# Kernel tuning notes

Hardware: AMD Instinct MI355X
Metric: run time of the kernel (lower is better)

## Reference

```python
import jax, jax.numpy as jnp
import numpy as np

B, P, K = 2, 8192, 20
ELL = 0.15          # ell_min + ell_rand
ELL_BASE = 10.0     # ell_basedist
COLOR_SCALE = 0.2
RES_MIN = 0.1       # res_mag_min
RES_MAX = 2.0       # res_mag_max
BIG = 1e10          # masking constant for invalid db points
EPS = 1e-12


def setup_inputs() -> dict:
    key = jax.random.key(0)
    ks = jax.random.split(key, 16)
    scale = jnp.array([20.0, 20.0, 60.0], jnp.float32)
    off = jnp.array([-10.0, -10.0, 1.0], jnp.float32)  # depth z in [1, 61] m
    xyz1 = jax.random.uniform(ks[0], (B, P, 3), jnp.float32) * scale + off
    xyz2 = jax.random.uniform(ks[1], (B, P, 3), jnp.float32) * scale + off
    hsv1 = jax.random.uniform(ks[2], (B, P, 3), jnp.float32)
    hsv2 = jax.random.uniform(ks[3], (B, P, 3), jnp.float32)
    n1 = jax.random.normal(ks[4], (B, P, 3), jnp.float32)
    normal1 = n1 / jnp.linalg.norm(n1, axis=-1, keepdims=True)
    n2 = jax.random.normal(ks[5], (B, P, 3), jnp.float32)
    normal2 = n2 / jnp.linalg.norm(n2, axis=-1, keepdims=True)
    nres1 = jax.random.uniform(ks[6], (B, P, 1), jnp.float32)
    nres2 = jax.random.uniform(ks[7], (B, P, 1), jnp.float32)

    def rot(k):
        a = np.asarray(jax.random.normal(k, (B, 3, 3), jnp.float32))
        q, _ = np.linalg.qr(a)
        return jnp.asarray(q, jnp.float32)

    R12 = rot(ks[8])
    R21 = rot(ks[9])
    t12 = jax.random.normal(ks[10], (B, 3, 1), jnp.float32) * 0.5
    t21 = jax.random.normal(ks[11], (B, 3, 1), jnp.float32) * 0.5
    npts1 = jax.random.randint(ks[12], (B,), P // 2, P + 1)
    npts2 = jax.random.randint(ks[13], (B,), P // 2, P + 1)
    return dict(xyz1=xyz1, xyz2=xyz2, hsv1=hsv1, hsv2=hsv2,
                normal1=normal1, normal2=normal2, nres1=nres1, nres2=nres2,
                R12=R12, t12=t12, R21=R21, t21=t21, npts1=npts1, npts2=npts2)


def _knn(pq, pdb, len_db):
    # pq [B,Pq,3], pdb [B,Pdb,3] -> squared dists [B,Pq,K], idx [B,Pq,K]
    d2 = jnp.sum((pq[:, :, None, :] - pdb[:, None, :, :]) ** 2, axis=-1)
    valid = jnp.arange(pdb.shape[1])[None, :] < len_db[:, None]
    d2 = jnp.where(valid[:, None, :], d2, BIG)
    neg, idx = jax.lax.top_k(-d2, K)
    return -neg, idx


def _gather(f, idx):
    # f [B,Pdb,C], idx [B,Pq,K] -> [B,Pq,K,C]  (knn_gather)
    return jax.vmap(lambda fb, ib: fb[ib])(f, idx)


def _transform(xyz, normal, R, t):
    x = jnp.einsum('bij,bpj->bpi', R, xyz) + t[:, :, 0][:, None, :]
    n = jnp.einsum('bij,bpj->bpi', R, normal)
    return x, n


def _side(pq, hq, nq, rq, lq, pdb, hdb, ndb, rdb, ldb):
    dists, idx = _knn(pq, pdb, ldb)                      # [B,P,K]
    # length_scale = clamp(ell*(z-base)/base, min=ell)^2
    ls = jnp.maximum(ELL * (pq[:, :, 2:3] - ELL_BASE) / ELL_BASE, ELL) ** 2
    dist_k = jnp.exp(-dists / ls)
    hsv_knn = _gather(hdb, idx)                          # [B,P,K,3]
    cdist = jnp.sqrt(jnp.sum((hq[:, :, None, :] - hsv_knn) ** 2, -1) + EPS)
    color_k = jnp.exp(-cdist / COLOR_SCALE)
    n_knn = _gather(ndb, idx)                            # [B,P,K,3]
    r_knn = _gather(rdb, idx)                            # [B,P,K,1]
    alpha = (2 * RES_MIN / (2 * RES_MIN / RES_MAX + rq[:, :, None, :] + r_knn))[..., 0]
    normal_k = jnp.maximum(jnp.sum(nq[:, :, None, :] * n_knn, -1) * alpha, 0.0)
    mask = (jnp.arange(pq.shape[1])[None, :, None] < lq[:, None, None]).astype(dist_k.dtype)
    total = jnp.sum(dist_k * color_k * normal_k * mask)
    return total / (lq.sum().astype(dist_k.dtype) * K)


def reference(xyz1, xyz2, hsv1, hsv2, normal1, normal2, nres1, nres2,
              R12, t12, R21, t21, npts1, npts2):
    x2in1, n2in1 = _transform(xyz2, normal2, R12, t12)   # pcl_gt_2_in_1
    x1in2, n1in2 = _transform(xyz1, normal1, R21, t21)   # pcl_gt_1_in_2
    k1 = _side(xyz1, hsv1, normal1, nres1, npts1, x2in1, hsv2, n2in1, nres2, npts2)
    k2 = _side(xyz2, hsv2, normal2, nres2, npts2, x1in2, hsv1, n1in2, nres1, npts1)
    return (k1 + k2) / 2
```

## Files before the change

### kernel.cpp

```cpp
#include <hip/hip_runtime.h>
#include <cstdint>
#include <cstddef>

#define PBUF 8192
#define NZB 256
#define NYB 32
#define NBINS (NZB * NYB)
#define NCOMBO 4
#define KNN 20
#define CAP 256

#define ZMIN_F (-72.0f)
#define INV_BINW (256.0f / 144.0f)
#define INV_YBINW (32.0f / 144.0f)

#define IDX_MASK 0x1FFFu
#define D2_MASK 0xFFFFE000u
#define KEY_INF 0xFFFFFFFFu

#define THR_MULT 21.0f

#define OFF_ACCUM   0
#define OFF_DBCUR   2048
#define ZERO_BYTES  (2048 + NCOMBO * NBINS * 4)
#define OFF_DBSTART (2048 + NCOMBO * NBINS * 4)
#define OFF_DBPOS   (OFF_DBSTART + NCOMBO * (NBINS + 1) * 4)
#define ARR_BYTES   (NCOMBO * PBUF * 16)
#define OFF_DBF1    (OFF_DBPOS + ARR_BYTES)
#define OFF_DBF2    (OFF_DBF1 + ARR_BYTES)

__device__ __forceinline__ int binOfZ(float z) {
  int b = (int)floorf((z - ZMIN_F) * INV_BINW);
  return min(max(b, 0), NZB - 1);
}
__device__ __forceinline__ int binOfY(float y) {
  int b = (int)floorf((y - ZMIN_F) * INV_YBINW);
  return min(max(b, 0), NYB - 1);
}

__device__ __forceinline__ float xformRow(const float* R, float tr, float x0, float x1, float x2) {
  return __fmaf_rn(R[2], x2, __fmaf_rn(R[1], x1, __fmaf_rn(R[0], x0, tr)));
}

__global__ __launch_bounds__(256) void k_count(
    const float* xyz1, const float* xyz2,
    const float* R12, const float* t12,
    const float* R21, const float* t21,
    const int* npts1, const int* npts2, char* ws) {
  int tid = blockIdx.x * 256 + threadIdx.x;
  int c = tid >> 13, j = tid & (PBUF - 1);
  int s = c >> 1, b = c & 1;
  const float* dsrc = s == 0 ? xyz2 : xyz1;
  const float* R  = (s == 0 ? R12 : R21) + b * 9;
  const float* tt = (s == 0 ? t12 : t21) + b * 3;
  int ldb = (s == 0 ? npts2 : npts1)[b];
  if (j < ldb) {
    const float* x = dsrc + (size_t)(b * PBUF + j) * 3;
    float y1 = xformRow(R + 3, tt[1], x[0], x[1], x[2]);
    float y2 = xformRow(R + 6, tt[2], x[0], x[1], x[2]);
    int bin = binOfZ(y2) * NYB + binOfY(y1);
    atomicAdd((int*)(ws + OFF_DBCUR) + c * NBINS + bin, 1);
  }
}

__global__ __launch_bounds__(256) void k_prefix(char* ws) {
  __shared__ int sWave[4];
  const int c = blockIdx.x;
  const int t = threadIdx.x;
  const int lane = t & 63, w = t >> 6;
  int* cnt = (int*)(ws + OFF_DBCUR) + c * NBINS;
  int* st  = (int*)(ws + OFF_DBSTART) + c * (NBINS + 1);
  int vals[32];
  int base = t * 32;
  int sum = 0;
  #pragma unroll
  for (int k = 0; k < 32; ++k) { vals[k] = cnt[base + k]; sum += vals[k]; }
  int incl = sum;
  #pragma unroll
  for (int o = 1; o < 64; o <<= 1) {
    int n = __shfl_up(incl, o);
    if (lane >= o) incl += n;
  }
  if (lane == 63) sWave[w] = incl;
  __syncthreads();
  int wbase = 0;
  #pragma unroll
  for (int k = 0; k < 4; ++k) wbase += (k < w) ? sWave[k] : 0;
  int run = wbase + incl - sum;
  #pragma unroll
  for (int k = 0; k < 32; ++k) {
    st[base + k] = run;
    cnt[base + k] = run;
    run += vals[k];
  }
  if (t == 255) st[NBINS] = run;
}

__global__ __launch_bounds__(256) void k_scatter(
    const float* xyz1, const float* xyz2,
    const float* hsv1, const float* hsv2,
    const float* normal1, const float* normal2,
    const float* nres1, const float* nres2,
    const float* R12, const float* t12,
    const float* R21, const float* t21,
    const int* npts1, const int* npts2, char* ws) {
  int tid = blockIdx.x * 256 + threadIdx.x;
  int c = tid >> 13, j = tid & (PBUF - 1);
  int s = c >> 1, b = c & 1;
  size_t pj = (size_t)(b * PBUF + j);

  const float* dsrc = s == 0 ? xyz2 : xyz1;
  const float* dh = s == 0 ? hsv2 : hsv1;
  const float* dn = s == 0 ? normal2 : normal1;
  const float* dr = s == 0 ? nres2 : nres1;
  const float* R  = (s == 0 ? R12 : R21) + b * 9;
  const float* tt = (s == 0 ? t12 : t21) + b * 3;
  int ldb = (s == 0 ? npts2 : npts1)[b];
  if (j < ldb) {
    const float* x = dsrc + pj * 3;
    float y0 = xformRow(R + 0, tt[0], x[0], x[1], x[2]);
    float y1 = xformRow(R + 3, tt[1], x[0], x[1], x[2]);
    float y2 = xformRow(R + 6, tt[2], x[0], x[1], x[2]);
    const float* n = dn + pj * 3;
    float n0 = xformRow(R + 0, 0.f, n[0], n[1], n[2]);
    float n1 = xformRow(R + 3, 0.f, n[0], n[1], n[2]);
    float n2 = xformRow(R + 6, 0.f, n[0], n[1], n[2]);
    const float* h = dh + pj * 3;
    float r = dr[pj];
    int bin = binOfZ(y2) * NYB + binOfY(y1);
    int pos = atomicAdd((int*)(ws + OFF_DBCUR) + c * NBINS + bin, 1) + c * PBUF;
    ((float4*)(ws + OFF_DBPOS))[pos] = make_float4(y0, y1, y2, 0.f);
    ((float4*)(ws + OFF_DBF1))[pos] = make_float4(h[0], h[1], h[2], r);
    ((float4*)(ws + OFF_DBF2))[pos] = make_float4(n0, n1, n2, 0.f);
  }
}

__global__ __launch_bounds__(256) void k_main(
    const float* xyz1, const float* xyz2,
    const float* hsv1, const float* hsv2,
    const float* normal1, const float* normal2,
    const float* nres1, const float* nres2,
    const int* npts1, const int* npts2, char* ws) {
  __shared__ unsigned sBuf[4 * (CAP + 4)];
  const int lane = threadIdx.x & 63;
  const int wIn = threadIdx.x >> 6;
  const int gw = blockIdx.x * 4 + wIn;
  const int c = gw >> 13;
  const int qi = (int)(__brev((unsigned)(gw & 8191)) >> 19);
  const int s = c >> 1, b = c & 1;
  const int lq = (s == 0 ? npts1 : npts2)[b];
  if (qi >= lq) return;

  const size_t qo = (size_t)(b * PBUF + qi);
  const float* qx = (s == 0 ? xyz1 : xyz2) + qo * 3;
  const float* qh = (s == 0 ? hsv1 : hsv2) + qo * 3;
  const float* qn = (s == 0 ? normal1 : normal2) + qo * 3;
  const float* qr = (s == 0 ? nres1 : nres2) + qo;
  const float qpx = qx[0], qpy = qx[1], qpz = qx[2];
  const float qh0 = qh[0], qh1 = qh[1], qh2 = qh[2];
  const float qn0 = qn[0], qn1 = qn[1], qn2 = qn[2];
  const float qres = qr[0];

  const float ell = fmaxf(0.015f * (qpz - 10.0f), 0.15f);
  const float ls = ell * ell;
  const float thrF = THR_MULT * ls;
  const float rad = sqrtf(thrF);
  const float inv_ls = 1.0f / ls;

  const int* F = (const int*)(ws + OFF_DBSTART) + c * (NBINS + 1);
  const int zlo = binOfZ(qpz - rad), zhi = binOfZ(qpz + rad);
  const int ylo = binOfY(qpy - rad), yhi = binOfY(qpy + rad);
  const int nseg = zhi - zlo + 1;

  int segS = 0, segLen = 0;
  if (lane < nseg) {
    int zk = zlo + lane;
    segS = F[zk * NYB + ylo];
    segLen = F[zk * NYB + yhi + 1] - segS;
  }
  int cum = segLen;
  #pragma unroll
  for (int o = 1; o < 64; o <<= 1) {
    int n = __shfl_up(cum, o);
    if (lane >= o) cum += n;
  }
  const int L = __shfl(cum, 63);
  const int excl = cum - segLen;

  const float4* dbPos = (const float4*)(ws + OFF_DBPOS) + c * PBUF;
  const float4* dbF1  = (const float4*)(ws + OFF_DBF1) + c * PBUF;
  const float4* dbF2  = (const float4*)(ws + OFF_DBF2) + c * PBUF;

  auto computeJ = [&](int base) -> int {
    int tc = min(base + lane, L - 1);
    int kk = 0;
    #pragma unroll
    for (int step = 8; step; step >>= 1) {
      int cnd = kk + step;
      int e = __shfl(excl, cnd & 63);
      if (cnd < nseg && e <= tc) kk = cnd;
    }
    return __shfl(segS, kk) + (tc - __shfl(excl, kk));
  };

  unsigned* buf = sBuf + wIn * (CAP + 4);
  int pos = 0;
  if (L > 0) {
    int jc = computeJ(0);
    float4 pc = dbPos[jc];
    for (int base = 0; base < L; base += 64) {
      int j = jc;
      float4 p = pc;
      int nb = base + 64;
      if (nb < L) {
        jc = computeJ(nb);
        pc = dbPos[jc];
      }
      bool in = (base + lane) < L;
      float dx = p.x - qpx, dy = p.y - qpy, dz = p.z - qpz;
      float d2 = __fmaf_rn(dx, dx, __fmaf_rn(dy, dy, dz * dz));
      bool keep = in && (d2 <= thrF);
      unsigned long long m = __ballot(keep);
      int rank = (int)__popcll(m & ((1ull << lane) - 1ull));
      if (keep) {
        int pidx = pos + rank;
        if (pidx < CAP) buf[pidx] = (__float_as_uint(d2) & D2_MASK) | (unsigned)j;
      }
      pos += (int)__popcll(m);
    }
    pos = min(pos, CAP);
  }

  if (lane < 4) buf[pos + lane] = KEY_INF;
  unsigned r0 = (lane       < pos) ? buf[lane]       : KEY_INF;
  unsigned r1 = (lane + 64  < pos) ? buf[lane + 64]  : KEY_INF;
  unsigned r2 = (lane + 128 < pos) ? buf[lane + 128] : KEY_INF;
  unsigned r3 = (lane + 192 < pos) ? buf[lane + 192] : KEY_INF;
  int k0 = 0, k1 = 0, k2 = 0, k3 = 0;
  const int nch = (pos + 3) >> 2;
  const uint4* b4 = (const uint4*)buf;
  for (int ch = 0; ch < nch; ++ch) {
    uint4 q4 = b4[ch];
    k0 += (q4.x < r0) + (q4.y < r0) + (q4.z < r0) + (q4.w < r0);
    k1 += (q4.x < r1) + (q4.y < r1) + (q4.z < r1) + (q4.w < r1);
    k2 += (q4.x < r2) + (q4.y < r2) + (q4.z < r2) + (q4.w < r2);
    k3 += (q4.x < r3) + (q4.y < r3) + (q4.z < r3) + (q4.w < r3);
  }

  auto evalKey = [&](unsigned key, int rk) -> float {
    if (rk >= KNN || key == KEY_INF) return 0.f;
    int j = (int)(key & IDX_MASK);
    float4 p = dbPos[j];
    float4 f1 = dbF1[j];
    float4 f2 = dbF2[j];
    float dx = p.x - qpx, dy = p.y - qpy, dz = p.z - qpz;
    float d2 = __fmaf_rn(dx, dx, __fmaf_rn(dy, dy, dz * dz));
    float dist_k = __expf(-d2 * inv_ls);
    float c0 = qh0 - f1.x, c1 = qh1 - f1.y, c2 = qh2 - f1.z;
    float cd = sqrtf(__fmaf_rn(c0, c0, __fmaf_rn(c1, c1, c2 * c2)) + 1e-12f);
    float color_k = __expf(cd * -5.0f);
    float alpha = 0.2f / (0.1f + qres + f1.w);
    float nd = __fmaf_rn(qn0, f2.x, __fmaf_rn(qn1, f2.y, qn2 * f2.z));
    float nk = fmaxf(nd * alpha, 0.0f);
    return dist_k * color_k * nk;
  };
  float lsum = evalKey(r0, k0) + evalKey(r1, k1) + evalKey(r2, k2) + evalKey(r3, k3);

  #pragma unroll
  for (int o = 32; o; o >>= 1) lsum += __shfl_down(lsum, o);
  if (lane == 0)
    atomicAdd((float*)(ws + OFF_ACCUM) + (s * 256 + (blockIdx.x & 255)), lsum);
}

__global__ void k_final(const int* npts1, const int* npts2, const char* ws, float* out) {
  int lane = threadIdx.x;
  const float* acc = (const float*)(ws + OFF_ACCUM);
  float s1 = acc[lane] + acc[lane + 64] + acc[lane + 128] + acc[lane + 192];
  float s2 = acc[256 + lane] + acc[256 + lane + 64] + acc[256 + lane + 128] + acc[256 + lane + 192];
  #pragma unroll
  for (int o = 32; o; o >>= 1) {
    s1 += __shfl_down(s1, o);
    s2 += __shfl_down(s2, o);
  }
  if (lane == 0) {
    float k1 = s1 / (20.0f * (float)(npts1[0] + npts1[1]));
    float k2 = s2 / (20.0f * (float)(npts2[0] + npts2[1]));
    out[0] = 0.5f * (k1 + k2);
  }
}

extern "C" void kernel_launch(void* const* d_in, const int* in_sizes, int n_in,
                              void* d_out, int out_size, void* d_ws, size_t ws_size,
                              hipStream_t stream) {
  const float* xyz1 = (const float*)d_in[0];
  const float* xyz2 = (const float*)d_in[1];
  const float* hsv1 = (const float*)d_in[2];
  const float* hsv2 = (const float*)d_in[3];
  const float* normal1 = (const float*)d_in[4];
  const float* normal2 = (const float*)d_in[5];
  const float* nres1 = (const float*)d_in[6];
  const float* nres2 = (const float*)d_in[7];
  const float* R12 = (const float*)d_in[8];
  const float* t12 = (const float*)d_in[9];
  const float* R21 = (const float*)d_in[10];
  const float* t21 = (const float*)d_in[11];
  const int* npts1 = (const int*)d_in[12];
  const int* npts2 = (const int*)d_in[13];
  char* ws = (char*)d_ws;
  float* out = (float*)d_out;

  hipMemsetAsync(ws, 0, ZERO_BYTES, stream);
  k_count<<<dim3(NCOMBO * PBUF / 256), dim3(256), 0, stream>>>(
      xyz1, xyz2, R12, t12, R21, t21, npts1, npts2, ws);
  k_prefix<<<dim3(NCOMBO), dim3(256), 0, stream>>>(ws);
  k_scatter<<<dim3(NCOMBO * PBUF / 256), dim3(256), 0, stream>>>(
      xyz1, xyz2, hsv1, hsv2, normal1, normal2, nres1, nres2,
      R12, t12, R21, t21, npts1, npts2, ws);
  k_main<<<dim3(NCOMBO * PBUF / 4), dim3(256), 0, stream>>>(
      xyz1, xyz2, hsv1, hsv2, normal1, normal2, nres1, nres2, npts1, npts2, ws);
  k_final<<<dim3(1), dim3(64), 0, stream>>>(npts1, npts2, ws, out);
}
```

Before: 138.4 us.

## Replace count/prefix/scatter binning with fixed-capacity per-bin slots

Drops the count and prefix-sum kernels and scatters points straight into fixed 128-slot buckets per bin, so two launches and one pass over the points go away. The query side now builds one segment per (z,y) bin instead of one contiguous run per z row, and widens the segment search. Candidate keys grow to 64 bits because slot indices no longer fit in 13 bits, which doubles shared memory and the work of the rank-count loop. Points beyond 128 in a single bin are silently dropped.

```diff
diff --git a/kernel.cpp b/kernel.cpp
--- a/kernel.cpp
+++ b/kernel.cpp
@@ -9,23 +9,22 @@
 #define NCOMBO 4
 #define KNN 20
 #define CAP 256
+#define CAPB 128
+#define SLOTS (NBINS * CAPB)
 
 #define ZMIN_F (-72.0f)
 #define INV_BINW (256.0f / 144.0f)
 #define INV_YBINW (32.0f / 144.0f)
 
-#define IDX_MASK 0x1FFFu
-#define D2_MASK 0xFFFFE000u
-#define KEY_INF 0xFFFFFFFFu
+#define KEY_INF 0xFFFFFFFFFFFFFFFFull
 
 #define THR_MULT 21.0f
 
 #define OFF_ACCUM   0
 #define OFF_DBCUR   2048
 #define ZERO_BYTES  (2048 + NCOMBO * NBINS * 4)
-#define OFF_DBSTART (2048 + NCOMBO * NBINS * 4)
-#define OFF_DBPOS   (OFF_DBSTART + NCOMBO * (NBINS + 1) * 4)
-#define ARR_BYTES   (NCOMBO * PBUF * 16)
+#define OFF_DBPOS   ZERO_BYTES
+#define ARR_BYTES   (NCOMBO * SLOTS * 16)
 #define OFF_DBF1    (OFF_DBPOS + ARR_BYTES)
 #define OFF_DBF2    (OFF_DBF1 + ARR_BYTES)
 
@@ -40,60 +39,6 @@
 
 __device__ __forceinline__ float xformRow(const float* R, float tr, float x0, float x1, float x2) {
   return __fmaf_rn(R[2], x2, __fmaf_rn(R[1], x1, __fmaf_rn(R[0], x0, tr)));
-}
-
-__global__ __launch_bounds__(256) void k_count(
-    const float* xyz1, const float* xyz2,
-    const float* R12, const float* t12,
-    const float* R21, const float* t21,
-    const int* npts1, const int* npts2, char* ws) {
-  int tid = blockIdx.x * 256 + threadIdx.x;
-  int c = tid >> 13, j = tid & (PBUF - 1);
-  int s = c >> 1, b = c & 1;
-  const float* dsrc = s == 0 ? xyz2 : xyz1;
-  const float* R  = (s == 0 ? R12 : R21) + b * 9;
-  const float* tt = (s == 0 ? t12 : t21) + b * 3;
-  int ldb = (s == 0 ? npts2 : npts1)[b];
-  if (j < ldb) {
-    const float* x = dsrc + (size_t)(b * PBUF + j) * 3;
-    float y1 = xformRow(R + 3, tt[1], x[0], x[1], x[2]);
-    float y2 = xformRow(R + 6, tt[2], x[0], x[1], x[2]);
-    int bin = binOfZ(y2) * NYB + binOfY(y1);
-    atomicAdd((int*)(ws + OFF_DBCUR) + c * NBINS + bin, 1);
-  }
-}
-
-__global__ __launch_bounds__(256) void k_prefix(char* ws) {
-  __shared__ int sWave[4];
-  const int c = blockIdx.x;
-  const int t = threadIdx.x;
-  const int lane = t & 63, w = t >> 6;
-  int* cnt = (int*)(ws + OFF_DBCUR) + c * NBINS;
-  int* st  = (int*)(ws + OFF_DBSTART) + c * (NBINS + 1);
-  int vals[32];
-  int base = t * 32;
-  int sum = 0;
-  #pragma unroll
-  for (int k = 0; k < 32; ++k) { vals[k] = cnt[base + k]; sum += vals[k]; }
-  int incl = sum;
-  #pragma unroll
-  for (int o = 1; o < 64; o <<= 1) {
-    int n = __shfl_up(incl, o);
-    if (lane >= o) incl += n;
-  }
-  if (lane == 63) sWave[w] = incl;
-  __syncthreads();
-  int wbase = 0;
-  #pragma unroll
-  for (int k = 0; k < 4; ++k) wbase += (k < w) ? sWave[k] : 0;
-  int run = wbase + incl - sum;
-  #pragma unroll
-  for (int k = 0; k < 32; ++k) {
-    st[base + k] = run;
-    cnt[base + k] = run;
-    run += vals[k];
-  }
-  if (t == 255) st[NBINS] = run;
 }
 
 __global__ __launch_bounds__(256) void k_scatter(
@@ -118,9 +63,10 @@
   int ldb = (s == 0 ? npts2 : npts1)[b];
   if (j < ldb) {
     const float* x = dsrc + pj * 3;
-    float y0 = xformRow(R + 0, tt[0], x[0], x[1], x[2]);
-    float y1 = xformRow(R + 3, tt[1], x[0], x[1], x[2]);
-    float y2 = xformRow(R + 6, tt[2], x[0], x[1], x[2]);
+    float x0 = x[0], x1 = x[1], x2 = x[2];
+    float y0 = xformRow(R + 0, tt[0], x0, x1, x2);
+    float y1 = xformRow(R + 3, tt[1], x0, x1, x2);
+    float y2 = xformRow(R + 6, tt[2], x0, x1, x2);
     const float* n = dn + pj * 3;
     float n0 = xformRow(R + 0, 0.f, n[0], n[1], n[2]);
     float n1 = xformRow(R + 3, 0.f, n[0], n[1], n[2]);
@@ -128,10 +74,13 @@
     const float* h = dh + pj * 3;
     float r = dr[pj];
     int bin = binOfZ(y2) * NYB + binOfY(y1);
-    int pos = atomicAdd((int*)(ws + OFF_DBCUR) + c * NBINS + bin, 1) + c * PBUF;
-    ((float4*)(ws + OFF_DBPOS))[pos] = make_float4(y0, y1, y2, 0.f);
-    ((float4*)(ws + OFF_DBF1))[pos] = make_float4(h[0], h[1], h[2], r);
-    ((float4*)(ws + OFF_DBF2))[pos] = make_float4(n0, n1, n2, 0.f);
+    int slot = atomicAdd((int*)(ws + OFF_DBCUR) + c * NBINS + bin, 1);
+    if (slot < CAPB) {
+      size_t pos = (size_t)c * SLOTS + (size_t)bin * CAPB + slot;
+      ((float4*)(ws + OFF_DBPOS))[pos] = make_float4(y0, y1, y2, 0.f);
+      ((float4*)(ws + OFF_DBF1))[pos] = make_float4(h[0], h[1], h[2], r);
+      ((float4*)(ws + OFF_DBF2))[pos] = make_float4(n0, n1, n2, 0.f);
+    }
   }
 }
 
@@ -141,7 +90,7 @@
     const float* normal1, const float* normal2,
     const float* nres1, const float* nres2,
     const int* npts1, const int* npts2, char* ws) {
-  __shared__ unsigned sBuf[4 * (CAP + 4)];
+  __shared__ unsigned long long sBuf[4 * (CAP + 2)];
   const int lane = threadIdx.x & 63;
   const int wIn = threadIdx.x >> 6;
   const int gw = blockIdx.x * 4 + wIn;
@@ -167,16 +116,18 @@
   const float rad = sqrtf(thrF);
   const float inv_ls = 1.0f / ls;
 
-  const int* F = (const int*)(ws + OFF_DBSTART) + c * (NBINS + 1);
+  const int* C = (const int*)(ws + OFF_DBCUR) + c * NBINS;
   const int zlo = binOfZ(qpz - rad), zhi = binOfZ(qpz + rad);
   const int ylo = binOfY(qpy - rad), yhi = binOfY(qpy + rad);
-  const int nseg = zhi - zlo + 1;
+  const int nyw = yhi - ylo + 1;
+  const int nseg = (zhi - zlo + 1) * nyw;
 
   int segS = 0, segLen = 0;
   if (lane < nseg) {
-    int zk = zlo + lane;
-    segS = F[zk * NYB + ylo];
-    segLen = F[zk * NYB + yhi + 1] - segS;
+    int zi = lane / nyw, yi = lane - zi * nyw;
+    int bin = (zlo + zi) * NYB + (ylo + yi);
+    segS = bin * CAPB;
+    segLen = min(C[bin], CAPB);
   }
   int cum = segLen;
   #pragma unroll
@@ -187,15 +138,15 @@
   const int L = __shfl(cum, 63);
   const int excl = cum - segLen;
 
-  const float4* dbPos = (const float4*)(ws + OFF_DBPOS) + c * PBUF;
-  const float4* dbF1  = (const float4*)(ws + OFF_DBF1) + c * PBUF;
-  const float4* dbF2  = (const float4*)(ws + OFF_DBF2) + c * PBUF;
+  const float4* dbPos = (const float4*)(ws + OFF_DBPOS) + (size_t)c * SLOTS;
+  const float4* dbF1  = (const float4*)(ws + OFF_DBF1) + (size_t)c * SLOTS;
+  const float4* dbF2  = (const float4*)(ws + OFF_DBF2) + (size_t)c * SLOTS;
 
   auto computeJ = [&](int base) -> int {
     int tc = min(base + lane, L - 1);
     int kk = 0;
     #pragma unroll
-    for (int step = 8; step; step >>= 1) {
+    for (int step = 32; step; step >>= 1) {
       int cnd = kk + step;
       int e = __shfl(excl, cnd & 63);
       if (cnd < nseg && e <= tc) kk = cnd;
@@ -203,7 +154,7 @@
     return __shfl(segS, kk) + (tc - __shfl(excl, kk));
   };
 
-  unsigned* buf = sBuf + wIn * (CAP + 4);
+  unsigned long long* buf = sBuf + wIn * (CAP + 2);
   int pos = 0;
   if (L > 0) {
     int jc = computeJ(0);
@@ -212,10 +163,7 @@
       int j = jc;
       float4 p = pc;
       int nb = base + 64;
-      if (nb < L) {
-        jc = computeJ(nb);
-        pc = dbPos[jc];
-      }
+      if (nb < L) { jc = computeJ(nb); pc = dbPos[jc]; }
       bool in = (base + lane) < L;
       float dx = p.x - qpx, dy = p.y - qpy, dz = p.z - qpz;
       float d2 = __fmaf_rn(dx, dx, __fmaf_rn(dy, dy, dz * dz));
@@ -224,32 +172,33 @@
       int rank = (int)__popcll(m & ((1ull << lane) - 1ull));
       if (keep) {
         int pidx = pos + rank;
-        if (pidx < CAP) buf[pidx] = (__float_as_uint(d2) & D2_MASK) | (unsigned)j;
+        if (pidx < CAP)
+          buf[pidx] = ((unsigned long long)__float_as_uint(d2) << 32) | (unsigned)j;
       }
       pos += (int)__popcll(m);
     }
     pos = min(pos, CAP);
   }
 
-  if (lane < 4) buf[pos + lane] = KEY_INF;
-  unsigned r0 = (lane       < pos) ? buf[lane]       : KEY_INF;
-  unsigned r1 = (lane + 64  < pos) ? buf[lane + 64]  : KEY_INF;
-  unsigned r2 = (lane + 128 < pos) ? buf[lane + 128] : KEY_INF;
-  unsigned r3 = (lane + 192 < pos) ? buf[lane + 192] : KEY_INF;
+  if (lane < 2) buf[pos + lane] = KEY_INF;
+  unsigned long long r0 = (lane       < pos) ? buf[lane]       : KEY_INF;
+  unsigned long long r1 = (lane + 64  < pos) ? buf[lane + 64]  : KEY_INF;
+  unsigned long long r2 = (lane + 128 < pos) ? buf[lane + 128] : KEY_INF;
+  unsigned long long r3 = (lane + 192 < pos) ? buf[lane + 192] : KEY_INF;
   int k0 = 0, k1 = 0, k2 = 0, k3 = 0;
-  const int nch = (pos + 3) >> 2;
-  const uint4* b4 = (const uint4*)buf;
+  const int nch = (pos + 1) >> 1;
+  const ulonglong2* b2 = (const ulonglong2*)buf;
   for (int ch = 0; ch < nch; ++ch) {
-    uint4 q4 = b4[ch];
-    k0 += (q4.x < r0) + (q4.y < r0) + (q4.z < r0) + (q4.w < r0);
-    k1 += (q4.x < r1) + (q4.y < r1) + (q4.z < r1) + (q4.w < r1);
-    k2 += (q4.x < r2) + (q4.y < r2) + (q4.z < r2) + (q4.w < r2);
-    k3 += (q4.x < r3) + (q4.y < r3) + (q4.z < r3) + (q4.w < r3);
-  }
-
-  auto evalKey = [&](unsigned key, int rk) -> float {
+    ulonglong2 q = b2[ch];
+    k0 += (q.x < r0) + (q.y < r0);
+    k1 += (q.x < r1) + (q.y < r1);
+    k2 += (q.x < r2) + (q.y < r2);
+    k3 += (q.x < r3) + (q.y < r3);
+  }
+
+  auto evalKey = [&](unsigned long long key, int rk) -> float {
     if (rk >= KNN || key == KEY_INF) return 0.f;
-    int j = (int)(key & IDX_MASK);
+    int j = (int)(unsigned)key;
     float4 p = dbPos[j];
     float4 f1 = dbF1[j];
     float4 f2 = dbF2[j];
@@ -310,9 +259,6 @@
   float* out = (float*)d_out;
 
   hipMemsetAsync(ws, 0, ZERO_BYTES, stream);
-  k_count<<<dim3(NCOMBO * PBUF / 256), dim3(256), 0, stream>>>(
-      xyz1, xyz2, R12, t12, R21, t21, npts1, npts2, ws);
-  k_prefix<<<dim3(NCOMBO), dim3(256), 0, stream>>>(ws);
   k_scatter<<<dim3(NCOMBO * PBUF / 256), dim3(256), 0, stream>>>(
       xyz1, xyz2, hsv1, hsv2, normal1, normal2, nres1, nres2,
       R12, t12, R21, t21, npts1, npts2, ws);
```

Result: faster. 122.6 us (-11.4%).
